# Performance work log

Hardware: AMD Instinct MI355X
Metric: run time of the kernel (lower is better)

The kernel has to match this reference:

```python
import jax, jax.numpy as jnp
import numpy as np

IMG_W, IMG_H = 416.0, 416.0
NUM_CLASSES = 80
NUM_ANCH = 3
LABEL_SMOOTH = 0.0
IGNORE_THR = 0.5
EPS = 1e-7


def _iou_cxcywh(b1, b2):
    # boxes (cx,cy,w,h); broadcasting IoU
    b1_min = b1[..., :2] - b1[..., 2:4] * 0.5
    b1_max = b1[..., :2] + b1[..., 2:4] * 0.5
    b2_min = b2[..., :2] - b2[..., 2:4] * 0.5
    b2_max = b2[..., :2] + b2[..., 2:4] * 0.5
    inter_wh = jnp.clip(jnp.minimum(b1_max, b2_max) - jnp.maximum(b1_min, b2_min), 0.0)
    inter = inter_wh[..., 0] * inter_wh[..., 1]
    a1 = b1[..., 2] * b1[..., 3]
    a2 = b2[..., 2] * b2[..., 3]
    return inter / jnp.maximum(a1 + a2 - inter, EPS)


def _ciou(b1, b2):
    iou = _iou_cxcywh(b1, b2)
    center_d = jnp.sum((b1[..., :2] - b2[..., :2]) ** 2, -1)
    enc_min = jnp.minimum(b1[..., :2] - b1[..., 2:4] * 0.5, b2[..., :2] - b2[..., 2:4] * 0.5)
    enc_max = jnp.maximum(b1[..., :2] + b1[..., 2:4] * 0.5, b2[..., :2] + b2[..., 2:4] * 0.5)
    diag = jnp.sum((enc_max - enc_min) ** 2, -1)
    ciou = iou - center_d / jnp.maximum(diag, EPS)
    v = (4.0 / (np.pi ** 2)) * (jnp.arctan(b1[..., 2] / jnp.maximum(b1[..., 3], EPS))
                                - jnp.arctan(b2[..., 2] / jnp.maximum(b2[..., 3], EPS))) ** 2
    alpha = v / jnp.maximum(1.0 - iou + v, EPS)
    return ciou - alpha * v


def _decode_level(feat, anch_wh):
    # head_process for one level: sigmoid xy + grid, exp wh * anchor, sigmoid conf
    bs, ch, H, W = feat.shape
    A = anch_wh.shape[0]
    f = feat.reshape(bs, A, ch // A, H, W).transpose(0, 3, 4, 1, 2)  # [bs,H,W,A,5+C]
    sx, sy = IMG_W / W, IMG_H / H
    gx = jnp.arange(W, dtype=feat.dtype)[None, :, None]
    gy = jnp.arange(H, dtype=feat.dtype)[:, None, None]
    px = (jax.nn.sigmoid(f[..., 0]) + gx) * sx
    py = (jax.nn.sigmoid(f[..., 1]) + gy) * sy
    pw = jnp.exp(f[..., 2]) * anch_wh[:, 0]
    ph = jnp.exp(f[..., 3]) * anch_wh[:, 1]
    box = jnp.stack([px, py, pw, ph], -1).reshape(bs, H * W * A, 4)
    conf = jax.nn.sigmoid(f[..., 4]).reshape(bs, H * W * A)
    cls = f[..., 5:].reshape(bs, H * W * A, NUM_CLASSES)
    # anchor prior boxes at every cell, same (y,x,a) flatten order
    acx = jnp.broadcast_to((gx + 0.5) * sx, (H, W, A))
    acy = jnp.broadcast_to((gy + 0.5) * sy, (H, W, A))
    aw = jnp.broadcast_to(anch_wh[:, 0], (H, W, A))
    ah = jnp.broadcast_to(anch_wh[:, 1], (H, W, A))
    priors = jnp.stack([acx, acy, aw, ah], -1).reshape(H * W * A, 4)
    return box, conf, cls, priors


def _forward(feats0, feats1, feats2, targets, anchors_shape):
    feats = [feats0, feats1, feats2]
    bs, n_t = targets.shape[0], targets.shape[1]
    boxes, confs, clss, priors, sizes, offs = [], [], [], [], [], []
    off = 0
    for i, f in enumerate(feats):
        aw = anchors_shape[i * NUM_ANCH:(i + 1) * NUM_ANCH]
        b, c, cl, pr = _decode_level(f, aw)
        boxes.append(b); confs.append(c); clss.append(cl); priors.append(pr)
        H, W = f.shape[2], f.shape[3]
        sizes.append((W, H)); offs.append(off); off += H * W * NUM_ANCH
    pred_box = jnp.concatenate(boxes, 1)      # [bs, total, 4]
    conf = jnp.concatenate(confs, 1)          # [bs, total]
    pred_cls = jnp.concatenate(clss, 1)       # [bs, total, C]
    anchors_all = jnp.concatenate(priors, 0)  # [total, 4]
    total = pred_box.shape[1]

    # ---- match_obj: best anchor shape per target via wh-only IoU ----
    tw, th = targets[..., 2], targets[..., 3]
    aw_, ah_ = anchors_shape[:, 0], anchors_shape[:, 1]
    inter = jnp.minimum(tw[..., None], aw_) * jnp.minimum(th[..., None], ah_)
    shape_iou = inter / jnp.maximum(tw[..., None] * th[..., None] + aw_ * ah_ - inter, EPS)
    best = jnp.argmax(shape_iou, -1)          # [bs, n_t]
    level = best // NUM_ANCH
    a = (best % NUM_ANCH).astype(jnp.int32)
    fs = jnp.array(sizes, dtype=jnp.int32)    # [3, (W,H)]
    offs_arr = jnp.array(offs, dtype=jnp.int32)
    Wl = fs[level, 0].astype(targets.dtype)
    Hl = fs[level, 1].astype(targets.dtype)
    X = jnp.clip(jnp.floor(targets[..., 0] / IMG_W * Wl), 0, Wl - 1).astype(jnp.int32)
    Y = jnp.clip(jnp.floor(targets[..., 1] / IMG_H * Hl), 0, Hl - 1).astype(jnp.int32)
    flat = offs_arr[level] + (Y * fs[level, 0] + X) * NUM_ANCH + a
    bidx = jnp.broadcast_to(jnp.arange(bs)[:, None], (bs, n_t))
    tidx = jnp.arange(bs * n_t, dtype=jnp.int32).reshape(bs, n_t)
    obj_mask = jnp.full((bs, total), -1, jnp.int32).at[bidx, flat].set(tidx)
    noobj_mask = jnp.ones((bs, total), jnp.int32).at[bidx, flat].set(0)

    # ---- match_noobj: ignore priors overlapping any GT above threshold ----
    iou_tn = _iou_cxcywh(targets[:, :, None, :4], anchors_all[None, None, :, :])  # [bs,n_t,total]
    max_iou = jnp.max(iou_tn, 1)
    noobj_mask = jnp.where(max_iou > IGNORE_THR, 0, noobj_mask)

    # ---- confidence BCE ----
    obj_labels = (obj_mask >= 0).astype(conf.dtype)
    p = jnp.clip(conf, EPS, 1.0 - EPS)
    bce = -(obj_labels * jnp.log(p) + (1.0 - obj_labels) * jnp.log(1.0 - p))
    loss_conf = jnp.sum(bce * obj_labels) + jnp.sum(bce * noobj_mask.astype(conf.dtype))

    # ---- localization (CIoU) + classification (smoothed log-softmax) on positives ----
    pos = obj_labels
    tsel = targets.reshape(bs * n_t, 5)[jnp.clip(obj_mask, 0)]  # [bs,total,5]
    tb = tsel[..., :4]
    scale = 2.0 - tb[..., 2] / IMG_W * tb[..., 3] / IMG_H
    loss_loc = jnp.sum((1.0 - _ciou(pred_box, tb)) * scale * pos)
    logsm = jax.nn.log_softmax(pred_cls, -1)
    labels = tsel[..., 4].astype(jnp.int32)
    picked = jnp.take_along_axis(logsm, labels[..., None], -1)[..., 0]
    s = LABEL_SMOOTH
    cls_nll = -((1.0 - s) * picked + (s / NUM_CLASSES) * jnp.sum(logsm, -1))
    loss_cls = jnp.sum(cls_nll * pos)

    return (loss_conf + loss_cls + loss_loc) / bs


def setup_inputs():
    key = jax.random.key(0)
    ks = jax.random.split(key, 6)
    bs, n_t = 32, 20
    ch = NUM_ANCH * (5 + NUM_CLASSES)  # 255
    feats0 = jax.random.normal(ks[0], (bs, ch, 13, 13), jnp.float32) * 0.1
    feats1 = jax.random.normal(ks[1], (bs, ch, 26, 26), jnp.float32) * 0.1
    feats2 = jax.random.normal(ks[2], (bs, ch, 52, 52), jnp.float32) * 0.1
    cxy = jax.random.uniform(ks[3], (bs, n_t, 2), jnp.float32, 8.0, 408.0)
    wh = jax.random.uniform(ks[4], (bs, n_t, 2), jnp.float32, 8.0, 120.0)
    cls = jax.random.randint(ks[5], (bs, n_t, 1), 0, NUM_CLASSES).astype(jnp.float32)
    targets = jnp.concatenate([cxy, wh, cls], -1)  # (cx,cy,w,h,class) in pixels
    anchors_shape = jnp.array([[116, 90], [156, 198], [373, 326],
                               [30, 61], [62, 45], [59, 119],
                               [10, 13], [16, 30], [33, 23]], jnp.float32)
    return {"feats0": feats0, "feats1": feats1, "feats2": feats2,
            "targets": targets, "anchors_shape": anchors_shape}


def reference(feats0, feats1, feats2, targets, anchors_shape):
    return _forward(feats0, feats1, feats2, targets, anchors_shape)
```

## Files before the change

### kernel.cpp

```cpp
#include <hip/hip_runtime.h>
#include <math.h>

#define NUM_CLASSES 80
#define EPSF 1e-7f

constexpr int BS = 32;
constexpr int NT = 20;
constexpr int TOTAL_CELLS = 169 + 676 + 2704;
constexpr int TOTAL_POS   = TOTAL_CELLS * 3;
constexpr int CONF_BLKS_PER_B = (TOTAL_POS + 255) / 256;
constexpr int CONF_BLKS = CONF_BLKS_PER_B * BS;
constexpr int POS_BLKS  = (BS * NT) / 4;
constexpr int NBLK = CONF_BLKS + POS_BLKS;

__device__ __forceinline__ float sigmoidf_(float x) {
    return 1.0f / (1.0f + expf(-x));
}

__device__ __forceinline__ int target_flat(float tx, float ty, float tw, float th,
                                           const float* anch) {
    int best = 0; float bestv = -1.0f;
    #pragma unroll
    for (int k = 0; k < 9; ++k) {
        float aw = anch[2 * k], ah = anch[2 * k + 1];
        float inter = fminf(tw, aw) * fminf(th, ah);
        float v = inter / fmaxf(tw * th + aw * ah - inter, EPSF);
        if (v > bestv) { bestv = v; best = k; }
    }
    int lvl = best / 3, a = best - lvl * 3;
    int Wl  = (lvl == 0) ? 13 : ((lvl == 1) ? 26 : 52);
    int off = (lvl == 0) ? 0  : ((lvl == 1) ? 507 : 2535);
    float Wf = (float)Wl;
    int X = (int)floorf(tx / 416.0f * Wf);
    int Y = (int)floorf(ty / 416.0f * Wf);
    X = min(max(X, 0), Wl - 1);
    Y = min(max(Y, 0), Wl - 1);
    return off + (Y * Wl + X) * 3 + a;
}

__global__ __launch_bounds__(256) void yolo_fused(
    const float* __restrict__ f0, const float* __restrict__ f1,
    const float* __restrict__ f2, const float* __restrict__ tgt,
    const float* __restrict__ anch, double* __restrict__ part)
{
    __shared__ double s_red[256];
    const int bi  = blockIdx.x;
    const int tid = threadIdx.x;
    double lsum = 0.0;

    if (bi < CONF_BLKS) {
        __shared__ float s_t[NT][5];
        __shared__ float s_anch[18];
        __shared__ int   s_flat[NT];
        const int b   = bi / CONF_BLKS_PER_B;
        const int sub = bi - b * CONF_BLKS_PER_B;

        if (tid < NT * 5) ((float*)s_t)[tid] = tgt[b * NT * 5 + tid];
        if (tid >= 128 && tid < 128 + 18) s_anch[tid - 128] = anch[tid - 128];
        __syncthreads();
        if (tid < NT)
            s_flat[tid] = target_flat(s_t[tid][0], s_t[tid][1], s_t[tid][2], s_t[tid][3], s_anch);
        __syncthreads();

        const int idx = sub * 256 + tid;
        if (idx < TOTAL_POS) {
            const int a    = idx / TOTAL_CELLS;
            const int cell = idx - a * TOTAL_CELLS;
            int lvl, W, cell0, posoff;
            const float* __restrict__ fb;
            if (cell < 169)      { lvl = 0; W = 13; cell0 = 0;   posoff = 0;    fb = f0; }
            else if (cell < 845) { lvl = 1; W = 26; cell0 = 169; posoff = 507;  fb = f1; }
            else                 { lvl = 2; W = 52; cell0 = 845; posoff = 2535; fb = f2; }
            const int HW  = W * W;
            const int rel = cell - cell0;
            const int y   = rel / W;
            const int x   = rel - y * W;
            const int pos = posoff + rel * 3 + a;

            const float cl = fb[((size_t)b * 255 + a * 85 + 4) * HW + rel];
            float p = sigmoidf_(cl);
            p = fminf(fmaxf(p, EPSF), 1.0f - EPSF);

            bool assigned = false;
            #pragma unroll
            for (int n = 0; n < NT; ++n) assigned |= (s_flat[n] == pos);

            if (assigned) {
                lsum = -(double)logf(p);
            } else {
                const float sxy = 416.0f / (float)W;
                const float acx = ((float)x + 0.5f) * sxy;
                const float acy = ((float)y + 0.5f) * sxy;
                const float aw  = s_anch[(lvl * 3 + a) * 2];
                const float ah  = s_anch[(lvl * 3 + a) * 2 + 1];
                const float anx = acx - aw * 0.5f, axx = acx + aw * 0.5f;
                const float any_ = acy - ah * 0.5f, axy = acy + ah * 0.5f;
                const float aarea = aw * ah;
                float mx = 0.0f;
                #pragma unroll 4
                for (int n = 0; n < NT; ++n) {
                    float tbx = s_t[n][0], tby = s_t[n][1];
                    float tbw = s_t[n][2], tbh = s_t[n][3];
                    float iw = fmaxf(fminf(axx, tbx + tbw * 0.5f) - fmaxf(anx, tbx - tbw * 0.5f), 0.0f);
                    float ih = fmaxf(fminf(axy, tby + tbh * 0.5f) - fmaxf(any_, tby - tbh * 0.5f), 0.0f);
                    float inter = iw * ih;
                    mx = fmaxf(mx, inter / fmaxf(aarea + tbw * tbh - inter, EPSF));
                }
                if (!(mx > 0.5f)) lsum = -(double)logf(1.0f - p);
            }
        }
    } else {
        const int wv   = (bi - CONF_BLKS) * 4 + (tid >> 6);
        const int lane = tid & 63;
        const int b = wv / NT;
        const int t = wv - b * NT;

        float an[18];
        #pragma unroll
        for (int k = 0; k < 18; ++k) an[k] = anch[k];

        int my_flat = 0x7fffffff;
        if (lane < NT) {
            const float* tp = tgt + ((size_t)b * NT + lane) * 5;
            my_flat = target_flat(tp[0], tp[1], tp[2], tp[3], an);
        }
        const int flat_t = __shfl(my_flat, t);
        bool winner = true;
        for (int n = t + 1; n < NT; ++n)
            if (__shfl(my_flat, n) == flat_t) winner = false;

        if (winner) {
            int lvl, W, off;
            const float* __restrict__ fb;
            if (flat_t < 507)       { lvl = 0; W = 13; off = 0;    fb = f0; }
            else if (flat_t < 2535) { lvl = 1; W = 26; off = 507;  fb = f1; }
            else                    { lvl = 2; W = 52; off = 2535; fb = f2; }
            const int HW  = W * W;
            const int rel = (flat_t - off) / 3;
            const int a   = flat_t - off - rel * 3;
            const int y   = rel / W;
            const int x   = rel - y * W;
            const float* f = fb + ((size_t)b * 255 + a * 85) * HW + rel;

            const float* tp = tgt + ((size_t)b * NT + t) * 5;
            const float tbx = tp[0], tby = tp[1], tbw = tp[2], tbh = tp[3];
            const int  label = (int)tp[4];

            const int c1 = lane;
            const int c2 = 64 + lane;
            const float lg1 = f[(size_t)(5 + c1) * HW];
            const float lg2 = (c2 < NUM_CLASSES) ? f[(size_t)(5 + c2) * HW] : -1e30f;
            float m = fmaxf(lg1, lg2);
            #pragma unroll
            for (int s = 32; s > 0; s >>= 1) m = fmaxf(m, __shfl_xor(m, s));
            float ssum = expf(lg1 - m) + ((c2 < NUM_CLASSES) ? expf(lg2 - m) : 0.0f);
            float pick = (c1 == label ? lg1 : 0.0f) + (c2 == label ? lg2 : 0.0f);
            #pragma unroll
            for (int s = 32; s > 0; s >>= 1) {
                ssum += __shfl_xor(ssum, s);
                pick += __shfl_xor(pick, s);
            }
            if (lane == 0) {
                lsum = -(double)(pick - m - logf(ssum));

                const float sxy = 416.0f / (float)W;
                const float aw = an[(lvl * 3 + a) * 2], ah = an[(lvl * 3 + a) * 2 + 1];
                float px = (sigmoidf_(f[0])              + (float)x) * sxy;
                float py = (sigmoidf_(f[(size_t)HW])     + (float)y) * sxy;
                float pw = expf(f[(size_t)2 * HW]) * aw;
                float ph = expf(f[(size_t)3 * HW]) * ah;

                float b1nx = px - pw * 0.5f, b1xx = px + pw * 0.5f;
                float b1ny = py - ph * 0.5f, b1xy = py + ph * 0.5f;
                float b2nx = tbx - tbw * 0.5f, b2xx = tbx + tbw * 0.5f;
                float b2ny = tby - tbh * 0.5f, b2xy = tby + tbh * 0.5f;
                float iw = fmaxf(fminf(b1xx, b2xx) - fmaxf(b1nx, b2nx), 0.0f);
                float ih = fmaxf(fminf(b1xy, b2xy) - fmaxf(b1ny, b2ny), 0.0f);
                float inter = iw * ih;
                float iou = inter / fmaxf(pw * ph + tbw * tbh - inter, EPSF);
                float cd = (px - tbx) * (px - tbx) + (py - tby) * (py - tby);
                float enx = fminf(b1nx, b2nx), exx = fmaxf(b1xx, b2xx);
                float eny = fminf(b1ny, b2ny), exy = fmaxf(b1xy, b2xy);
                float diag = (exx - enx) * (exx - enx) + (exy - eny) * (exy - eny);
                float ciou = iou - cd / fmaxf(diag, EPSF);
                float dA = atanf(pw / fmaxf(ph, EPSF)) - atanf(tbw / fmaxf(tbh, EPSF));
                float v = (4.0f / (float)(M_PI * M_PI)) * dA * dA;
                float alpha = v / fmaxf(1.0f - iou + v, EPSF);
                float scale = 2.0f - tbw / 416.0f * tbh / 416.0f;
                lsum += (double)((1.0f - (ciou - alpha * v)) * scale);
            }
        }
    }

    s_red[tid] = lsum;
    __syncthreads();
    for (int s = 128; s > 0; s >>= 1) {
        if (tid < s) s_red[tid] += s_red[tid + s];
        __syncthreads();
    }
    if (tid == 0) part[bi] = s_red[0];
}

__global__ __launch_bounds__(512) void yolo_finish(const double* __restrict__ part,
                                                   float* __restrict__ out)
{
    __shared__ double s[512];
    const int tid = threadIdx.x;
    double v = 0.0;
    for (int i = tid; i < NBLK; i += 512) v += part[i];
    s[tid] = v;
    __syncthreads();
    for (int st = 256; st > 0; st >>= 1) {
        if (tid < st) s[tid] += s[tid + st];
        __syncthreads();
    }
    if (tid == 0) out[0] = (float)(s[0] / (double)BS);
}

extern "C" void kernel_launch(void* const* d_in, const int* in_sizes, int n_in,
                              void* d_out, int out_size, void* d_ws, size_t ws_size,
                              hipStream_t stream) {
    const float* f0   = (const float*)d_in[0];
    const float* f1   = (const float*)d_in[1];
    const float* f2   = (const float*)d_in[2];
    const float* tgt  = (const float*)d_in[3];
    const float* anch = (const float*)d_in[4];
    double* part = (double*)d_ws;

    yolo_fused<<<NBLK, 256, 0, stream>>>(f0, f1, f2, tgt, anch, part);
    yolo_finish<<<1, 512, 0, stream>>>(part, (float*)d_out);
}
```

Measured before the change: 19.47 us.

## Fuse final reduction into main kernel via last-block atomic counter

Replaces the separate finish kernel with a last-block-done pattern: each block writes its partial and bumps an atomic counter, and the last block to arrive sums all partials and writes the output. The in-block reduction also moves from a shared-memory tree to wavefront shuffles. This removes one kernel launch and cuts the number of block barriers, but adds a memset launch for the counter and a serial tail on the last block.

```diff
diff --git a/kernel.cpp b/kernel.cpp
--- a/kernel.cpp
+++ b/kernel.cpp
@@ -41,9 +41,11 @@
 __global__ __launch_bounds__(256) void yolo_fused(
     const float* __restrict__ f0, const float* __restrict__ f1,
     const float* __restrict__ f2, const float* __restrict__ tgt,
-    const float* __restrict__ anch, double* __restrict__ part)
+    const float* __restrict__ anch, double* __restrict__ part,
+    unsigned int* __restrict__ counter, float* __restrict__ out)
 {
-    __shared__ double s_red[256];
+    __shared__ double s_w[4];
+    __shared__ bool   s_last;
     const int bi  = blockIdx.x;
     const int tid = threadIdx.x;
     double lsum = 0.0;
@@ -192,29 +194,28 @@
         }
     }
 
-    s_red[tid] = lsum;
+    #pragma unroll
+    for (int s = 32; s > 0; s >>= 1) lsum += __shfl_xor(lsum, s);
+    if ((tid & 63) == 0) s_w[tid >> 6] = lsum;
     __syncthreads();
-    for (int s = 128; s > 0; s >>= 1) {
-        if (tid < s) s_red[tid] += s_red[tid + s];
+    if (tid == 0) {
+        part[bi] = s_w[0] + s_w[1] + s_w[2] + s_w[3];
+        __threadfence();
+        s_last = (atomicAdd(counter, 1u) == NBLK - 1);
+        __threadfence();
+    }
+    __syncthreads();
+
+    if (s_last) {
+        const volatile double* vp = part;
+        double v = 0.0;
+        for (int i = tid; i < NBLK; i += 256) v += vp[i];
+        #pragma unroll
+        for (int s = 32; s > 0; s >>= 1) v += __shfl_xor(v, s);
+        if ((tid & 63) == 0) s_w[tid >> 6] = v;
         __syncthreads();
-    }
-    if (tid == 0) part[bi] = s_red[0];
-}
-
-__global__ __launch_bounds__(512) void yolo_finish(const double* __restrict__ part,
-                                                   float* __restrict__ out)
-{
-    __shared__ double s[512];
-    const int tid = threadIdx.x;
-    double v = 0.0;
-    for (int i = tid; i < NBLK; i += 512) v += part[i];
-    s[tid] = v;
-    __syncthreads();
-    for (int st = 256; st > 0; st >>= 1) {
-        if (tid < st) s[tid] += s[tid + st];
-        __syncthreads();
-    }
-    if (tid == 0) out[0] = (float)(s[0] / (double)BS);
+        if (tid == 0) out[0] = (float)((s_w[0] + s_w[1] + s_w[2] + s_w[3]) / (double)BS);
+    }
 }
 
 extern "C" void kernel_launch(void* const* d_in, const int* in_sizes, int n_in,
@@ -226,7 +227,8 @@
     const float* tgt  = (const float*)d_in[3];
     const float* anch = (const float*)d_in[4];
     double* part = (double*)d_ws;
-
-    yolo_fused<<<NBLK, 256, 0, stream>>>(f0, f1, f2, tgt, anch, part);
-    yolo_finish<<<1, 512, 0, stream>>>(part, (float*)d_out);
-}
+    unsigned int* counter = (unsigned int*)((char*)d_ws + NBLK * sizeof(double));
+
+    hipMemsetAsync(counter, 0, sizeof(unsigned int), stream);
+    yolo_fused<<<NBLK, 256, 0, stream>>>(f0, f1, f2, tgt, anch, part, counter, (float*)d_out);
+}
```

New measurement: 61.70 us. 217% more time.
